# Kernel optimization log

Measured on AMD Instinct MI355X. Metric: run time of the kernel, lower is better.

## Reference

```python
import jax, jax.numpy as jnp
import numpy as np

ALPHA = 0.25        # focal alpha
GAMMA = 2.0         # focal gamma
POS_T = 0.5         # max_iou positive threshold
NEG_T = 0.4         # max_iou negative threshold
SL1_BETA = 1.0 / 9.0  # smooth_l1 with sigma=3
EPS = 1e-6

N, T, A, C = 8, 64, 65536, 80


def setup_inputs() -> dict:
    key = jax.random.key(0)
    ks = jax.random.split(key, 6)
    labels = jax.random.randint(ks[0], (N, T), 1, C)
    y_true = jax.nn.one_hot(labels, C, dtype=jnp.float32)
    xy = jax.random.uniform(ks[1], (N, T, 2)) * 0.7
    wh = jax.random.uniform(ks[2], (N, T, 2)) * 0.25 + 0.02
    bbox_true = jnp.concatenate([xy, xy + wh], axis=-1)
    valid = (jnp.arange(T) < 24).astype(jnp.float32)  # zero-pad remaining GT rows
    bbox_true = bbox_true * valid[None, :, None]
    axy = jax.random.uniform(ks[3], (A, 2)) * 0.9
    awh = jax.random.uniform(jax.random.fold_in(ks[3], 1), (A, 2)) * 0.15 + 0.02
    anchors = jnp.concatenate([axy, axy + awh], axis=-1)
    y_pred = jax.random.normal(ks[4], (N, A, C), dtype=jnp.float32)
    bbox_pred = jax.random.normal(ks[5], (N, A, 4), dtype=jnp.float32) * 0.1
    return {"y_true": y_true, "bbox_true": bbox_true, "y_pred": y_pred,
            "bbox_pred": bbox_pred, "anchors": anchors}


def _iou(b1, b2):
    # b1: (T,4), b2: (A,4) -> (T,A)
    a1 = jnp.maximum(b1[:, 2] - b1[:, 0], 0) * jnp.maximum(b1[:, 3] - b1[:, 1], 0)
    a2 = jnp.maximum(b2[:, 2] - b2[:, 0], 0) * jnp.maximum(b2[:, 3] - b2[:, 1], 0)
    lt = jnp.maximum(b1[:, None, :2], b2[None, :, :2])
    rb = jnp.minimum(b1[:, None, 2:], b2[None, :, 2:])
    wh = jnp.maximum(rb - lt, 0.0)
    inter = wh[..., 0] * wh[..., 1]
    union = a1[:, None] + a2[None, :] - inter
    return inter / jnp.maximum(union, 1e-10)


def _bbox2delta(boxes, anchors):
    # standard (dx, dy, dw, dh) encoding, mean=0 / std=1
    wa = jnp.maximum(anchors[:, 2] - anchors[:, 0], EPS)
    ha = jnp.maximum(anchors[:, 3] - anchors[:, 1], EPS)
    cxa = anchors[:, 0] + 0.5 * wa
    cya = anchors[:, 1] + 0.5 * ha
    wt = jnp.maximum(boxes[:, 2] - boxes[:, 0], EPS)
    ht = jnp.maximum(boxes[:, 3] - boxes[:, 1], EPS)
    cxt = boxes[:, 0] + 0.5 * (boxes[:, 2] - boxes[:, 0])
    cyt = boxes[:, 1] + 0.5 * (boxes[:, 3] - boxes[:, 1])
    return jnp.stack([(cxt - cxa) / wa, (cyt - cya) / ha,
                      jnp.log(wt / wa), jnp.log(ht / ha)], axis=-1)


def _encode_target(y_true_i, bbox_true_i, anchors):
    # y_true_i: (T,C), bbox_true_i: (T,4), anchors: (A,4)
    valid = jnp.any(bbox_true_i > 0, axis=-1)                 # (T,)
    iou = jnp.where(valid[:, None], _iou(bbox_true_i, anchors), -1.0)  # (T,A)
    max_iou = iou.max(axis=0)                                  # (A,)
    assigned = iou.argmax(axis=0)                              # (A,) gt index per anchor
    pos = max_iou >= POS_T
    neg = (max_iou < NEG_T)
    # low-quality matching: each valid gt's best anchor is positive for that gt
    gt_best = iou.argmax(axis=1)                               # (T,)
    gt_best_iou = iou.max(axis=1)
    lq = valid & (gt_best_iou > 0)
    assigned = assigned.at[gt_best].set(jnp.where(lq, jnp.arange(bbox_true_i.shape[0]), assigned[gt_best]))
    pos = pos.at[gt_best].set(jnp.where(lq, True, pos[gt_best]))
    neg = neg & (~pos)
    state = jnp.where(pos, 1, jnp.where(neg, -1, 0)).astype(jnp.int8)[:, None]  # (A,1)
    # class target: background one-hot [1,0,...,0], positives get gt label
    bg = jnp.zeros((anchors.shape[0], y_true_i.shape[-1]), jnp.float32).at[:, 0].set(1.0)
    yt = jnp.where(pos[:, None], y_true_i[assigned], bg)       # (A,C)
    delta = _bbox2delta(bbox_true_i[assigned], anchors)        # (A,4)
    bt = jnp.where(pos[:, None], delta, 0.0)
    return state, yt, bt


def _focal_bce(y_true, logits):
    # elementwise sigmoid focal loss
    ce = jnp.maximum(logits, 0) - logits * y_true + jnp.log1p(jnp.exp(-jnp.abs(logits)))
    p = jax.nn.sigmoid(logits)
    p_t = y_true * p + (1.0 - y_true) * (1.0 - p)
    a_t = y_true * ALPHA + (1.0 - y_true) * (1.0 - ALPHA)
    return a_t * jnp.power(1.0 - p_t, GAMMA) * ce


def _smooth_l1(y_true, y_pred):
    d = jnp.abs(y_true - y_pred)
    return jnp.where(d < SL1_BETA, 0.5 * d * d / SL1_BETA, d - 0.5 * SL1_BETA)


def _sanitize(x):
    return jnp.where(jnp.isnan(x) | jnp.isinf(x), 0.0, x)


def reference(y_true, bbox_true, y_pred, bbox_pred, anchors):
    state, yt, bt = jax.vmap(lambda a, b: _encode_target(a, b, anchors))(y_true, bbox_true)
    positive_w = (state == 1).astype(y_pred.dtype)   # (N,A,1)
    target_w = (state != 0).astype(y_pred.dtype)     # (N,A,1)
    avg_factor = jnp.sum(jnp.maximum(jnp.sum(positive_w, axis=-2), 1.0))
    yt = yt * positive_w                              # background=False zeroes non-positives
    cls = jnp.sum(_focal_bce(yt, y_pred) * target_w) / avg_factor
    box = jnp.sum(_smooth_l1(bt, bbox_pred) * positive_w) / avg_factor
    return _sanitize(cls), _sanitize(box)
```

## Files before the change

kernel.cpp:

```cpp
#include <hip/hip_runtime.h>
#include <hip/hip_bf16.h>
#include <math.h>

#define NB 8
#define TB 64
#define AB 65536
#define CB 80
#define EPSF 1e-6f

#define LOSS_BLOCKS 2048
#define LOSS_ITERS  16

#define WS_CODE_OFF   4096
#define WS_PCLS_OFF   (4096 + NB*AB*4)
#define WS_PBOX_OFF   (WS_PCLS_OFF + LOSS_BLOCKS*4)
#define WS_PPOS_OFF   (WS_PBOX_OFF + LOSS_BLOCKS*4)

__global__ __launch_bounds__(256) void assign_kernel(
    const float* __restrict__ bbox_true,
    const float* __restrict__ anchors,
    int*   __restrict__ code,
    unsigned long long* __restrict__ gt_key)
{
    __shared__ float4 s_box[TB];
    __shared__ float  s_a1[TB];
    __shared__ unsigned long long s_key[TB];

    const int blk   = blockIdx.x;
    const int i     = blk >> 8;
    const int abase = (blk & 255) << 8;
    const int tid   = threadIdx.x;

    if (tid < TB) {
        float4 b = ((const float4*)bbox_true)[i * TB + tid];
        bool valid = (b.x > 0.f) || (b.y > 0.f) || (b.z > 0.f) || (b.w > 0.f);
        float a1 = fmaxf(b.z - b.x, 0.f) * fmaxf(b.w - b.y, 0.f);
        s_box[tid] = b;
        s_a1[tid]  = valid ? a1 : -1.0f;
        s_key[tid] = 0ull;
    }
    __syncthreads();

    const int a = abase + tid;
    const float4 an = ((const float4*)anchors)[a];
    const float a2 = fmaxf(an.z - an.x, 0.f) * fmaxf(an.w - an.y, 0.f);

    float best = -1.0f;
    int bestt = 0;
    #pragma unroll 8
    for (int t = 0; t < TB; ++t) {
        float a1 = s_a1[t];
        float iou = -1.0f;
        if (a1 >= 0.f) {
            float4 b = s_box[t];
            float lx = fmaxf(b.x, an.x), ly = fmaxf(b.y, an.y);
            float rx = fminf(b.z, an.z), ry = fminf(b.w, an.w);
            float w = fmaxf(rx - lx, 0.f), h = fmaxf(ry - ly, 0.f);
            float inter = w * h;
            float uni = a1 + a2 - inter;
            iou = inter / fmaxf(uni, 1e-10f);
            if (iou > 0.f) {
                unsigned long long key =
                    ((unsigned long long)__float_as_uint(iou) << 32) |
                    (unsigned long long)((unsigned)a ^ 0xFFFFFFFFu);
                if (key > s_key[t])
                    atomicMax(&s_key[t], key);
            }
        }
        if (iou > best) { best = iou; bestt = t; }
    }
    bool pos = best >= 0.5f;
    bool neg = best < 0.4f;
    code[i * AB + a] = pos ? bestt : (neg ? -1 : -2);

    __syncthreads();
    if (tid < TB) {
        unsigned long long k = s_key[tid];
        if (k) atomicMax(&gt_key[i * TB + tid], k);
    }
}

__global__ void lq_kernel(const unsigned long long* __restrict__ gt_key,
                          int* __restrict__ code)
{
    __shared__ unsigned long long sk[NB * TB];
    const int tid = threadIdx.x;
    sk[tid] = gt_key[tid];
    __syncthreads();
    const int i = tid >> 6, t = tid & 63;
    unsigned long long k = sk[tid];
    if (k) {
        unsigned a = (unsigned)(k & 0xFFFFFFFFull) ^ 0xFFFFFFFFu;
        bool win = true;
        for (int t2 = t + 1; t2 < TB; ++t2) {
            unsigned long long k2 = sk[(i << 6) | t2];
            if (k2 && (((unsigned)(k2 & 0xFFFFFFFFull) ^ 0xFFFFFFFFu) == a))
                win = false;
        }
        if (win) code[i * AB + (int)a] = t;
    }
}

__device__ __forceinline__ float focal1(bool ypos, float l) {
    float q  = __expf(-fabsf(l));
    float r  = __builtin_amdgcn_rcpf(1.f + q);
    float lg = __logf(r);
    float ce = fmaxf(l, 0.f) - (ypos ? l : 0.f) - lg;
    float p  = (l >= 0.f) ? r : 1.f - r;
    float pt = ypos ? p : 1.f - p;
    float at = ypos ? 0.25f : 0.75f;
    float om = 1.f - pt;
    return at * om * om * ce;
}
__device__ __forceinline__ float smooth_l1(float x) {
    float d = fabsf(x);
    return d < (1.f / 9.f) ? 4.5f * d * d : d - (0.5f / 9.f);
}

__global__ __launch_bounds__(320) void loss_kernel(
    const float* __restrict__ y_true,
    const float* __restrict__ bbox_true,
    const float* __restrict__ y_pred,
    const float* __restrict__ bbox_pred,
    const float* __restrict__ anchors,
    const int*   __restrict__ code,
    float* __restrict__ partial_cls,
    float* __restrict__ partial_box,
    int*   __restrict__ partial_pos)
{
    const int tid   = threadIdx.x;
    const int la    = tid / 20;
    const int chunk = tid % 20;
    const int b   = blockIdx.x;
    const int i   = b >> 8;
    const int sub = b & 255;

    const float4* yp4 = (const float4*)y_pred;
    const float4* yt4 = (const float4*)y_true;

    float cls_acc = 0.f, box_acc = 0.f;
    int posc = 0;

    #pragma unroll 2
    for (int it = 0; it < LOSS_ITERS; ++it) {
        const int a = sub * 16 + la + it * (256 * 16);
        const int g = i * AB + a;
        const int cv = code[g];
        float4 l4 = yp4[g * 20 + chunk];
        if (cv != -2) {
            bool pos = cv >= 0;
            float y0 = 0.f, y1 = 0.f, y2 = 0.f, y3 = 0.f;
            if (pos) {
                float4 yv = yt4[(i * TB + cv) * 20 + chunk];
                y0 = yv.x; y1 = yv.y; y2 = yv.z; y3 = yv.w;
            }
            cls_acc += focal1(y0 != 0.f, l4.x) + focal1(y1 != 0.f, l4.y) +
                       focal1(y2 != 0.f, l4.z) + focal1(y3 != 0.f, l4.w);
            if (pos && chunk == 0) {
                posc += 1;
                float4 bt = ((const float4*)bbox_true)[i * TB + cv];
                float4 an = ((const float4*)anchors)[a];
                float wa = fmaxf(an.z - an.x, EPSF), ha = fmaxf(an.w - an.y, EPSF);
                float cxa = an.x + 0.5f * wa,  cya = an.y + 0.5f * ha;
                float wt = fmaxf(bt.z - bt.x, EPSF), ht = fmaxf(bt.w - bt.y, EPSF);
                float cxt = bt.x + 0.5f * (bt.z - bt.x), cyt = bt.y + 0.5f * (bt.w - bt.y);
                float d0 = (cxt - cxa) / wa, d1 = (cyt - cya) / ha;
                float d2 = __logf(wt / wa),  d3 = __logf(ht / ha);
                float4 bp = ((const float4*)bbox_pred)[g];
                box_acc += smooth_l1(d0 - bp.x) + smooth_l1(d1 - bp.y) +
                           smooth_l1(d2 - bp.z) + smooth_l1(d3 - bp.w);
            }
        }
    }

    for (int off = 32; off > 0; off >>= 1) {
        cls_acc += __shfl_down(cls_acc, off);
        box_acc += __shfl_down(box_acc, off);
        posc    += __shfl_down(posc, off);
    }
    __shared__ float s_cls[5], s_box[5];
    __shared__ int   s_pc[5];
    int wave = tid >> 6, lane = tid & 63;
    if (lane == 0) { s_cls[wave] = cls_acc; s_box[wave] = box_acc; s_pc[wave] = posc; }
    __syncthreads();
    if (tid == 0) {
        partial_cls[b] = s_cls[0] + s_cls[1] + s_cls[2] + s_cls[3] + s_cls[4];
        partial_box[b] = s_box[0] + s_box[1] + s_box[2] + s_box[3] + s_box[4];
        partial_pos[b] = s_pc[0] + s_pc[1] + s_pc[2] + s_pc[3] + s_pc[4];
    }
}

__global__ __launch_bounds__(256) void reduce_kernel(
    const float* __restrict__ partial_cls,
    const float* __restrict__ partial_box,
    const int*   __restrict__ partial_pos,
    float* __restrict__ out)
{
    const int tid = threadIdx.x;
    const int wave = tid >> 6, lane = tid & 63;
    __shared__ double sc[4], sb[4];
    __shared__ int    si[4];
    __shared__ float  s_avg;

    double c = 0.0, bx = 0.0;
    #pragma unroll
    for (int j = 0; j < LOSS_BLOCKS / 256; ++j) {
        c  += (double)partial_cls[tid + j * 256];
        bx += (double)partial_box[tid + j * 256];
    }

    float avg = 0.f;
    for (int bb = 0; bb < NB; ++bb) {
        int p = partial_pos[bb * 256 + tid];
        for (int off = 32; off > 0; off >>= 1) p += __shfl_down(p, off);
        if (lane == 0) si[wave] = p;
        __syncthreads();
        if (tid == 0) {
            int tot = si[0] + si[1] + si[2] + si[3];
            avg += fmaxf((float)tot, 1.0f);
        }
        __syncthreads();
    }
    if (tid == 0) s_avg = avg;

    for (int off = 32; off > 0; off >>= 1) {
        c  += __shfl_down(c, off);
        bx += __shfl_down(bx, off);
    }
    if (lane == 0) { sc[wave] = c; sb[wave] = bx; }
    __syncthreads();
    if (tid == 0) {
        double ct = sc[0] + sc[1] + sc[2] + sc[3];
        double bt = sb[0] + sb[1] + sb[2] + sb[3];
        float cf = (float)(ct / (double)s_avg);
        float bf = (float)(bt / (double)s_avg);
        if (isnan(cf) || isinf(cf)) cf = 0.f;
        if (isnan(bf) || isinf(bf)) bf = 0.f;
        out[0] = cf;
        out[1] = bf;
    }
}

extern "C" void kernel_launch(void* const* d_in, const int* in_sizes, int n_in,
                              void* d_out, int out_size, void* d_ws, size_t ws_size,
                              hipStream_t stream) {
    const float* y_true    = (const float*)d_in[0];
    const float* bbox_true = (const float*)d_in[1];
    const float* y_pred    = (const float*)d_in[2];
    const float* bbox_pred = (const float*)d_in[3];
    const float* anchors   = (const float*)d_in[4];
    float* out = (float*)d_out;

    char* ws = (char*)d_ws;
    unsigned long long* gt_key = (unsigned long long*)ws;
    int*   code        = (int*)(ws + WS_CODE_OFF);
    float* partial_cls = (float*)(ws + WS_PCLS_OFF);
    float* partial_box = (float*)(ws + WS_PBOX_OFF);
    int*   partial_pos = (int*)(ws + WS_PPOS_OFF);

    hipMemsetAsync(ws, 0, NB * TB * sizeof(unsigned long long), stream);

    assign_kernel<<<NB * AB / 256, 256, 0, stream>>>(bbox_true, anchors, code, gt_key);
    lq_kernel<<<1, NB * TB, 0, stream>>>(gt_key, code);
    loss_kernel<<<LOSS_BLOCKS, 320, 0, stream>>>(
        y_true, bbox_true, y_pred, bbox_pred, anchors, code,
        partial_cls, partial_box, partial_pos);
    reduce_kernel<<<1, 256, 0, stream>>>(partial_cls, partial_box, partial_pos, out);
}
```

Before: 298.9 us.

## Fold low-quality match and final reduction into last-block tails; compact valid GTs

Removes the separate lq_kernel and reduce_kernel launches by having the last-finishing block of assign_kernel and loss_kernel, detected via an atomic counter, perform the low-quality match fixup and the final reduction. The assign loop now iterates only over compacted valid GT boxes found with a ballot, which skips the padded zero rows. This saves two launches and wasted IoU work in exchange for threadfences, counter atomics and a serialized tail in one block.

```diff
diff --git a/kernel.cpp b/kernel.cpp
--- a/kernel.cpp
+++ b/kernel.cpp
@@ -1,5 +1,4 @@
 #include <hip/hip_runtime.h>
-#include <hip/hip_bf16.h>
 #include <math.h>
 
 #define NB 8
@@ -11,20 +10,25 @@
 #define LOSS_BLOCKS 2048
 #define LOSS_ITERS  16
 
-#define WS_CODE_OFF   4096
-#define WS_PCLS_OFF   (4096 + NB*AB*4)
-#define WS_PBOX_OFF   (WS_PCLS_OFF + LOSS_BLOCKS*4)
-#define WS_PPOS_OFF   (WS_PBOX_OFF + LOSS_BLOCKS*4)
+#define WS_CNT_OFF   4096
+#define WS_CODE_OFF  4352
+#define WS_PCLS_OFF  (WS_CODE_OFF + NB*AB*4)
+#define WS_PBOX_OFF  (WS_PCLS_OFF + LOSS_BLOCKS*4)
+#define WS_PPOS_OFF  (WS_PBOX_OFF + LOSS_BLOCKS*4)
 
 __global__ __launch_bounds__(256) void assign_kernel(
     const float* __restrict__ bbox_true,
     const float* __restrict__ anchors,
     int*   __restrict__ code,
-    unsigned long long* __restrict__ gt_key)
+    unsigned long long* __restrict__ gt_key,
+    unsigned* __restrict__ cnt)
 {
     __shared__ float4 s_box[TB];
     __shared__ float  s_a1[TB];
+    __shared__ int    s_t[TB];
     __shared__ unsigned long long s_key[TB];
+    __shared__ int s_nv;
+    __shared__ unsigned s_rank;
 
     const int blk   = blockIdx.x;
     const int i     = blk >> 8;
@@ -34,40 +38,42 @@
     if (tid < TB) {
         float4 b = ((const float4*)bbox_true)[i * TB + tid];
         bool valid = (b.x > 0.f) || (b.y > 0.f) || (b.z > 0.f) || (b.w > 0.f);
-        float a1 = fmaxf(b.z - b.x, 0.f) * fmaxf(b.w - b.y, 0.f);
-        s_box[tid] = b;
-        s_a1[tid]  = valid ? a1 : -1.0f;
+        unsigned long long m = __ballot(valid);
+        int slot = __popcll(m & ((1ull << tid) - 1ull));
+        if (valid) {
+            s_box[slot] = b;
+            s_a1[slot]  = fmaxf(b.z - b.x, 0.f) * fmaxf(b.w - b.y, 0.f);
+            s_t[slot]   = tid;
+        }
         s_key[tid] = 0ull;
+        if (tid == 0) s_nv = __popcll(m);
     }
     __syncthreads();
 
     const int a = abase + tid;
     const float4 an = ((const float4*)anchors)[a];
     const float a2 = fmaxf(an.z - an.x, 0.f) * fmaxf(an.w - an.y, 0.f);
+    const unsigned long long inva = (unsigned long long)((unsigned)a ^ 0xFFFFFFFFu);
+    const int nv = s_nv;
 
     float best = -1.0f;
     int bestt = 0;
-    #pragma unroll 8
-    for (int t = 0; t < TB; ++t) {
-        float a1 = s_a1[t];
-        float iou = -1.0f;
-        if (a1 >= 0.f) {
-            float4 b = s_box[t];
-            float lx = fmaxf(b.x, an.x), ly = fmaxf(b.y, an.y);
-            float rx = fminf(b.z, an.z), ry = fminf(b.w, an.w);
-            float w = fmaxf(rx - lx, 0.f), h = fmaxf(ry - ly, 0.f);
-            float inter = w * h;
-            float uni = a1 + a2 - inter;
-            iou = inter / fmaxf(uni, 1e-10f);
-            if (iou > 0.f) {
-                unsigned long long key =
-                    ((unsigned long long)__float_as_uint(iou) << 32) |
-                    (unsigned long long)((unsigned)a ^ 0xFFFFFFFFu);
-                if (key > s_key[t])
-                    atomicMax(&s_key[t], key);
-            }
-        }
+    #pragma unroll 4
+    for (int j = 0; j < nv; ++j) {
+        float4 b = s_box[j];
+        float lx = fmaxf(b.x, an.x), ly = fmaxf(b.y, an.y);
+        float rx = fminf(b.z, an.z), ry = fminf(b.w, an.w);
+        float w = fmaxf(rx - lx, 0.f), h = fmaxf(ry - ly, 0.f);
+        float inter = w * h;
+        float uni = s_a1[j] + a2 - inter;
+        float iou = inter / fmaxf(uni, 1e-10f);
+        int t = s_t[j];
         if (iou > best) { best = iou; bestt = t; }
+        if (iou > 0.f) {
+            unsigned long long key = ((unsigned long long)__float_as_uint(iou) << 32) | inva;
+            if (key > s_key[t])
+                atomicMax(&s_key[t], key);
+        }
     }
     bool pos = best >= 0.5f;
     bool neg = best < 0.4f;
@@ -78,26 +84,32 @@
         unsigned long long k = s_key[tid];
         if (k) atomicMax(&gt_key[i * TB + tid], k);
     }
-}
-
-__global__ void lq_kernel(const unsigned long long* __restrict__ gt_key,
-                          int* __restrict__ code)
-{
-    __shared__ unsigned long long sk[NB * TB];
-    const int tid = threadIdx.x;
-    sk[tid] = gt_key[tid];
-    __syncthreads();
-    const int i = tid >> 6, t = tid & 63;
-    unsigned long long k = sk[tid];
-    if (k) {
-        unsigned a = (unsigned)(k & 0xFFFFFFFFull) ^ 0xFFFFFFFFu;
-        bool win = true;
-        for (int t2 = t + 1; t2 < TB; ++t2) {
-            unsigned long long k2 = sk[(i << 6) | t2];
-            if (k2 && (((unsigned)(k2 & 0xFFFFFFFFull) ^ 0xFFFFFFFFu) == a))
-                win = false;
-        }
-        if (win) code[i * AB + (int)a] = t;
+
+    __threadfence();
+    __syncthreads();
+    if (tid == 0) s_rank = atomicAdd(cnt, 1u);
+    __syncthreads();
+    if (s_rank == gridDim.x - 1) {
+        __shared__ unsigned long long sk[NB * TB];
+        for (int e = tid; e < NB * TB; e += 256)
+            sk[e] = __hip_atomic_load(&gt_key[e], __ATOMIC_RELAXED, __HIP_MEMORY_SCOPE_AGENT);
+        __syncthreads();
+        for (int e = tid; e < NB * TB; e += 256) {
+            unsigned long long k = sk[e];
+            if (k) {
+                int ii = e >> 6, t = e & 63;
+                unsigned aa = (unsigned)(k & 0xFFFFFFFFull) ^ 0xFFFFFFFFu;
+                bool win = true;
+                for (int t2 = t + 1; t2 < TB; ++t2) {
+                    unsigned long long k2 = sk[(ii << 6) | t2];
+                    if (k2 && (((unsigned)(k2 & 0xFFFFFFFFull) ^ 0xFFFFFFFFu) == aa))
+                        win = false;
+                }
+                if (win)
+                    __hip_atomic_store(&code[ii * AB + (int)aa], t,
+                                       __ATOMIC_RELAXED, __HIP_MEMORY_SCOPE_AGENT);
+            }
+        }
     }
 }
 
@@ -126,14 +138,16 @@
     const int*   __restrict__ code,
     float* __restrict__ partial_cls,
     float* __restrict__ partial_box,
-    int*   __restrict__ partial_pos)
+    int*   __restrict__ partial_pos,
+    unsigned* __restrict__ cnt,
+    float* __restrict__ out)
 {
     const int tid   = threadIdx.x;
     const int la    = tid / 20;
     const int chunk = tid % 20;
-    const int b   = blockIdx.x;
-    const int i   = b >> 8;
-    const int sub = b & 255;
+    const int blk = blockIdx.x;
+    const int i   = blk >> 8;
+    const int sub = blk & 255;
 
     const float4* yp4 = (const float4*)y_pred;
     const float4* yt4 = (const float4*)y_true;
@@ -178,66 +192,65 @@
         box_acc += __shfl_down(box_acc, off);
         posc    += __shfl_down(posc, off);
     }
-    __shared__ float s_cls[5], s_box[5];
+    __shared__ float s_cls[5], s_boxp[5];
     __shared__ int   s_pc[5];
-    int wave = tid >> 6, lane = tid & 63;
-    if (lane == 0) { s_cls[wave] = cls_acc; s_box[wave] = box_acc; s_pc[wave] = posc; }
+    __shared__ unsigned s_rank;
+    const int wave = tid >> 6, lane = tid & 63;
+    if (lane == 0) { s_cls[wave] = cls_acc; s_boxp[wave] = box_acc; s_pc[wave] = posc; }
     __syncthreads();
     if (tid == 0) {
-        partial_cls[b] = s_cls[0] + s_cls[1] + s_cls[2] + s_cls[3] + s_cls[4];
-        partial_box[b] = s_box[0] + s_box[1] + s_box[2] + s_box[3] + s_box[4];
-        partial_pos[b] = s_pc[0] + s_pc[1] + s_pc[2] + s_pc[3] + s_pc[4];
-    }
-}
-
-__global__ __launch_bounds__(256) void reduce_kernel(
-    const float* __restrict__ partial_cls,
-    const float* __restrict__ partial_box,
-    const int*   __restrict__ partial_pos,
-    float* __restrict__ out)
-{
-    const int tid = threadIdx.x;
-    const int wave = tid >> 6, lane = tid & 63;
-    __shared__ double sc[4], sb[4];
-    __shared__ int    si[4];
-    __shared__ float  s_avg;
-
-    double c = 0.0, bx = 0.0;
-    #pragma unroll
-    for (int j = 0; j < LOSS_BLOCKS / 256; ++j) {
-        c  += (double)partial_cls[tid + j * 256];
-        bx += (double)partial_box[tid + j * 256];
-    }
-
-    float avg = 0.f;
-    for (int bb = 0; bb < NB; ++bb) {
-        int p = partial_pos[bb * 256 + tid];
-        for (int off = 32; off > 0; off >>= 1) p += __shfl_down(p, off);
-        if (lane == 0) si[wave] = p;
+        float pc = s_cls[0] + s_cls[1] + s_cls[2] + s_cls[3] + s_cls[4];
+        float pb = s_boxp[0] + s_boxp[1] + s_boxp[2] + s_boxp[3] + s_boxp[4];
+        int   pp = s_pc[0] + s_pc[1] + s_pc[2] + s_pc[3] + s_pc[4];
+        __hip_atomic_store(&partial_cls[blk], pc, __ATOMIC_RELAXED, __HIP_MEMORY_SCOPE_AGENT);
+        __hip_atomic_store(&partial_box[blk], pb, __ATOMIC_RELAXED, __HIP_MEMORY_SCOPE_AGENT);
+        __hip_atomic_store(&partial_pos[blk], pp, __ATOMIC_RELAXED, __HIP_MEMORY_SCOPE_AGENT);
+        __threadfence();
+        s_rank = atomicAdd(cnt, 1u);
+    }
+    __syncthreads();
+
+    if (s_rank == LOSS_BLOCKS - 1) {
+        __threadfence();
+        __shared__ float  s_bc[NB];
+        __shared__ double sdc[4], sdb[4];
+        if (tid < 256) {
+            for (int bb = wave; bb < NB; bb += 4) {
+                int p = 0;
+                #pragma unroll
+                for (int j = 0; j < 4; ++j)
+                    p += __hip_atomic_load(&partial_pos[bb * 256 + lane + j * 64],
+                                           __ATOMIC_RELAXED, __HIP_MEMORY_SCOPE_AGENT);
+                for (int off = 32; off > 0; off >>= 1) p += __shfl_down(p, off);
+                if (lane == 0) s_bc[bb] = fmaxf((float)p, 1.0f);
+            }
+            double c = 0.0, bxs = 0.0;
+            #pragma unroll
+            for (int j = 0; j < 8; ++j) {
+                c   += (double)__hip_atomic_load(&partial_cls[tid + j * 256],
+                                                 __ATOMIC_RELAXED, __HIP_MEMORY_SCOPE_AGENT);
+                bxs += (double)__hip_atomic_load(&partial_box[tid + j * 256],
+                                                 __ATOMIC_RELAXED, __HIP_MEMORY_SCOPE_AGENT);
+            }
+            for (int off = 32; off > 0; off >>= 1) {
+                c   += __shfl_down(c, off);
+                bxs += __shfl_down(bxs, off);
+            }
+            if (lane == 0) { sdc[wave] = c; sdb[wave] = bxs; }
+        }
         __syncthreads();
         if (tid == 0) {
-            int tot = si[0] + si[1] + si[2] + si[3];
-            avg += fmaxf((float)tot, 1.0f);
-        }
-        __syncthreads();
-    }
-    if (tid == 0) s_avg = avg;
-
-    for (int off = 32; off > 0; off >>= 1) {
-        c  += __shfl_down(c, off);
-        bx += __shfl_down(bx, off);
-    }
-    if (lane == 0) { sc[wave] = c; sb[wave] = bx; }
-    __syncthreads();
-    if (tid == 0) {
-        double ct = sc[0] + sc[1] + sc[2] + sc[3];
-        double bt = sb[0] + sb[1] + sb[2] + sb[3];
-        float cf = (float)(ct / (double)s_avg);
-        float bf = (float)(bt / (double)s_avg);
-        if (isnan(cf) || isinf(cf)) cf = 0.f;
-        if (isnan(bf) || isinf(bf)) bf = 0.f;
-        out[0] = cf;
-        out[1] = bf;
+            double ct = sdc[0] + sdc[1] + sdc[2] + sdc[3];
+            double bt = sdb[0] + sdb[1] + sdb[2] + sdb[3];
+            float avg = 0.f;
+            for (int bb = 0; bb < NB; ++bb) avg += s_bc[bb];
+            float cf = (float)(ct / (double)avg);
+            float bf = (float)(bt / (double)avg);
+            if (isnan(cf) || isinf(cf)) cf = 0.f;
+            if (isnan(bf) || isinf(bf)) bf = 0.f;
+            out[0] = cf;
+            out[1] = bf;
+        }
     }
 }
 
@@ -253,17 +266,16 @@
 
     char* ws = (char*)d_ws;
     unsigned long long* gt_key = (unsigned long long*)ws;
+    unsigned* cnt      = (unsigned*)(ws + WS_CNT_OFF);
     int*   code        = (int*)(ws + WS_CODE_OFF);
     float* partial_cls = (float*)(ws + WS_PCLS_OFF);
     float* partial_box = (float*)(ws + WS_PBOX_OFF);
     int*   partial_pos = (int*)(ws + WS_PPOS_OFF);
 
-    hipMemsetAsync(ws, 0, NB * TB * sizeof(unsigned long long), stream);
-
-    assign_kernel<<<NB * AB / 256, 256, 0, stream>>>(bbox_true, anchors, code, gt_key);
-    lq_kernel<<<1, NB * TB, 0, stream>>>(gt_key, code);
+    hipMemsetAsync(ws, 0, WS_CNT_OFF + 2 * sizeof(unsigned), stream);
+
+    assign_kernel<<<NB * AB / 256, 256, 0, stream>>>(bbox_true, anchors, code, gt_key, cnt);
     loss_kernel<<<LOSS_BLOCKS, 320, 0, stream>>>(
         y_true, bbox_true, y_pred, bbox_pred, anchors, code,
-        partial_cls, partial_box, partial_pos);
-    reduce_kernel<<<1, 256, 0, stream>>>(partial_cls, partial_box, partial_pos, out);
-}
+        partial_cls, partial_box, partial_pos, cnt + 1, out);
+}
```

After: 483.7 us. +61.8%, slower.
